# Kernel optimization log

Hardware: AMD Instinct MI355X
Metric: run time of the kernel (lower is better)

## Reference

```python
import jax, jax.numpy as jnp
import numpy as np

DIM = 1024
DIM_QK = 1024
DIM_V = 1024
H = 16
SCALE = 1.0 / (DIM_QK ** 0.5)  # NOTE: module scales by sqrt(dim_qk), not sqrt(head_dim)


def setup_inputs() -> dict:
    key = jax.random.key(0)
    ks = jax.random.split(key, 12)
    B, S = 2, 2048
    q = jax.random.normal(ks[0], (B, S, DIM), jnp.float32)
    k = jax.random.normal(ks[1], (B, S, DIM), jnp.float32)
    v = jax.random.normal(ks[2], (B, S, DIM), jnp.float32)
    mask = jax.random.randint(ks[3], (B, 1, S, S), 0, 2) > 0  # True = masked
    s = 1.0 / np.sqrt(DIM)
    Wq = jax.random.uniform(ks[4], (DIM_QK, DIM), jnp.float32, -s, s)
    bq = jax.random.uniform(ks[5], (DIM_QK,), jnp.float32, -s, s)
    Wk = jax.random.uniform(ks[6], (DIM_QK, DIM), jnp.float32, -s, s)
    bk = jax.random.uniform(ks[7], (DIM_QK,), jnp.float32, -s, s)
    Wv = jax.random.uniform(ks[8], (DIM_V, DIM), jnp.float32, -s, s)
    bv = jax.random.uniform(ks[9], (DIM_V,), jnp.float32, -s, s)
    Wo = jax.random.uniform(ks[10], (DIM_V, DIM), jnp.float32, -s, s)
    bo = jax.random.uniform(ks[11], (DIM_V,), jnp.float32, -s, s)
    return {"q": q, "k": k, "v": v, "mask": mask,
            "Wq": Wq, "bq": bq, "Wk": Wk, "bk": bk,
            "Wv": Wv, "bv": bv, "Wo": Wo, "bo": bo}


def reference(q, k, v, mask, Wq, bq, Wk, bk, Wv, bv, Wo, bo):
    B, Sq, _ = q.shape
    Skv = k.shape[1]
    # projections (torch Linear: x @ W.T + b)
    qh = (q @ Wq.T + bq).reshape(B, Sq, H, DIM_QK // H).transpose(0, 2, 1, 3)   # [B,H,Sq,dk]
    kh = (k @ Wk.T + bk).reshape(B, Skv, H, DIM_QK // H).transpose(0, 2, 1, 3)  # [B,H,Skv,dk]
    vh = (v @ Wv.T + bv).reshape(B, Skv, H, DIM_V // H).transpose(0, 2, 1, 3)   # [B,H,Skv,dv]
    attn = jnp.einsum('bhqd,bhkd->bhqk', qh, kh) * SCALE
    attn = jnp.where(mask, jnp.float32(-1e20), attn)
    attn = jax.nn.softmax(attn, axis=-1)
    # dropout is identity in eval / p=0
    out = jnp.einsum('bhqk,bhkd->bhqd', attn, vh)            # [B,H,Sq,dv]
    out = out.transpose(0, 2, 1, 3).reshape(B, Sq, DIM_V)
    return out @ Wo.T + bo
```

## Files before the change

kernel.cpp:

```cpp
#include <hip/hip_runtime.h>
#include <hip/hip_bf16.h>

typedef __attribute__((ext_vector_type(8))) __bf16 bf16x8;
typedef __attribute__((ext_vector_type(4))) short short4v;
typedef __attribute__((ext_vector_type(4))) float f32x4;
typedef __attribute__((ext_vector_type(4))) unsigned int uint4v;
typedef __attribute__((ext_vector_type(2))) unsigned int uint2v;

#define S_LEN 2048
#define DIM_  1024
#define HDIM  64
#define SCALE2 0.045084441f

#define EXP2F(x) __builtin_amdgcn_exp2f(x)

#define ATTN_SWZ(row, col8) (((row) * 64) + (((col8) ^ ((row) & 7)) << 3))

__device__ __forceinline__ void async_copy16(const void* gp, void* lp) {
  __builtin_amdgcn_global_load_lds(
      (const __attribute__((address_space(1))) unsigned int*)gp,
      (__attribute__((address_space(3))) unsigned int*)lp, 16, 0, 0);
}

__device__ __forceinline__ unsigned f2bf_u(float f) {
  unsigned u = __builtin_bit_cast(unsigned, f);
  return (u + 0x7FFFu + ((u >> 16) & 1u)) >> 16;
}
__device__ __forceinline__ unsigned pack2(float a, float b) {
  return f2bf_u(a) | (f2bf_u(b) << 16);
}
__device__ __forceinline__ unsigned cvtpk(float a, float b) {
  float2 f; f.x = a; f.y = b;
  __hip_bfloat162 h = __float22bfloat162_rn(f);
  unsigned u;
  __builtin_memcpy(&u, &h, 4);
  return u;
}

__global__ __launch_bounds__(256) void cvt_kernel(
    const float* __restrict__ s0, const float* __restrict__ s1, const float* __restrict__ s2,
    const float* __restrict__ s3, const float* __restrict__ s4, const float* __restrict__ s5,
    const float* __restrict__ s6,
    __hip_bfloat16* __restrict__ d0, __hip_bfloat16* __restrict__ d1, __hip_bfloat16* __restrict__ d2,
    __hip_bfloat16* __restrict__ d3, __hip_bfloat16* __restrict__ d4, __hip_bfloat16* __restrict__ d5,
    __hip_bfloat16* __restrict__ d6,
    const int* __restrict__ mask, unsigned long long* __restrict__ bits)
{
  if (blockIdx.y == 7) {
    int wave = threadIdx.x >> 6, lane = threadIdx.x & 63;
    int gw = blockIdx.x * 4 + wave;
#pragma unroll
    for (int it = 0; it < 16; ++it) {
      int w = gw * 16 + it;
      int m = mask[(size_t)w * 64 + lane];
      unsigned long long bal = __ballot(m != 0);
      if (lane == 0) bits[w] = bal;
    }
    return;
  }
  const float* srcs[7] = {s0, s1, s2, s3, s4, s5, s6};
  __hip_bfloat16* dsts[7] = {d0, d1, d2, d3, d4, d5, d6};
  const int sizes[7] = {4194304, 4194304, 4194304, 1048576, 1048576, 1048576, 1048576};
  int rg = blockIdx.y;
  int base = (blockIdx.x * 256 + threadIdx.x) * 8;
  if (base >= sizes[rg]) return;
  const float* s = srcs[rg] + base;
  f32x4 a = *(const f32x4*)s;
  f32x4 b = *(const f32x4*)(s + 4);
  uint4v o;
  o.x = pack2(a[0], a[1]); o.y = pack2(a[2], a[3]);
  o.z = pack2(b[0], b[1]); o.w = pack2(b[2], b[3]);
  *(uint4v*)(dsts[rg] + base) = o;
}

__device__ __forceinline__ void swz(int r, int& m0, int& n0) {
  int c  = ((r & 7) << 2) | (r >> 6);
  int xl = (r >> 3) & 7;
  m0 = ((c >> 3) * 8 + xl) * 128;
  n0 = (c & 7) * 128;
}

__global__ __launch_bounds__(256) void qkv_gemm_kernel(
    const __hip_bfloat16* __restrict__ xq, const __hip_bfloat16* __restrict__ xk,
    const __hip_bfloat16* __restrict__ xv,
    const __hip_bfloat16* __restrict__ Wq, const float* __restrict__ bq,
    const __hip_bfloat16* __restrict__ Wk, const float* __restrict__ bk,
    const __hip_bfloat16* __restrict__ Wv, const float* __restrict__ bv,
    __hip_bfloat16* __restrict__ Q, __hip_bfloat16* __restrict__ Kk,
    __hip_bfloat16* __restrict__ VT)
{
  const __hip_bfloat16 *X, *W; const float* bias;
  if (blockIdx.z == 0)      { X = xq; W = Wq; bias = bq; }
  else if (blockIdx.z == 1) { X = xk; W = Wk; bias = bk; }
  else                      { X = xv; W = Wv; bias = bv; }

  constexpr int K = 1024, N = 1024;
  __shared__ alignas(16) __hip_bfloat16 As[2][128 * 32];
  __shared__ alignas(16) __hip_bfloat16 Bs[2][128 * 32];
  const int tid  = threadIdx.x;
  const int lane = tid & 63;
  const int wave = tid >> 6;
  const int t    = lane & 15;
  const int quad = lane >> 4;
  const int wm   = wave >> 1;
  const int wn   = wave & 1;
  int m0, n0;
  swz(blockIdx.x, m0, n0);

  f32x4 acc[4][4] = {};

  const int c0 = tid, c1 = 256 + tid;
  const int r0 = c0 >> 2, o0 = (c0 & 3) * 8;
  const int r1 = c1 >> 2, o1 = (c1 & 3) * 8;
  const __hip_bfloat16* xp0 = &X[(size_t)(m0 + r0) * K + o0];
  const __hip_bfloat16* xp1 = &X[(size_t)(m0 + r1) * K + o1];
  const __hip_bfloat16* wp0 = &W[(size_t)(n0 + r0) * K + o0];
  const __hip_bfloat16* wp1 = &W[(size_t)(n0 + r1) * K + o1];

  async_copy16(xp0, &As[0][c0 * 8]);
  async_copy16(xp1, &As[0][c1 * 8]);
  async_copy16(wp0, &Bs[0][c0 * 8]);
  async_copy16(wp1, &Bs[0][c1 * 8]);

  int buf = 0;
  for (int k0 = 0; k0 < K; k0 += 32) {
    __syncthreads();
    if (k0 + 32 < K) {
      int nb = buf ^ 1;
      int kn = k0 + 32;
      async_copy16(xp0 + kn, &As[nb][c0 * 8]);
      async_copy16(xp1 + kn, &As[nb][c1 * 8]);
      async_copy16(wp0 + kn, &Bs[nb][c0 * 8]);
      async_copy16(wp1 + kn, &Bs[nb][c1 * 8]);
    }
    bf16x8 a[4], b[4];
#pragma unroll
    for (int i = 0; i < 4; ++i)
      a[i] = *(const bf16x8*)&As[buf][(wm * 64 + i * 16 + t) * 32 + quad * 8];
#pragma unroll
    for (int j = 0; j < 4; ++j)
      b[j] = *(const bf16x8*)&Bs[buf][(wn * 64 + j * 16 + t) * 32 + quad * 8];
#pragma unroll
    for (int i = 0; i < 4; ++i)
#pragma unroll
      for (int j = 0; j < 4; ++j)
        acc[i][j] = __builtin_amdgcn_mfma_f32_16x16x32_bf16(a[i], b[j], acc[i][j], 0, 0, 0);
    buf ^= 1;
  }

  float bj[4];
#pragma unroll
  for (int j = 0; j < 4; ++j)
    bj[j] = bias[n0 + wn * 64 + j * 16 + t];

  if (blockIdx.z == 2) {
#pragma unroll
    for (int i = 0; i < 4; ++i)
#pragma unroll
      for (int j = 0; j < 4; ++j) {
        int m = m0 + wm * 64 + i * 16 + quad * 4;
        int n = n0 + wn * 64 + j * 16 + t;
        int bb = m >> 11, kv = m & 2047;
        int hh = n >> 6,  dv = n & 63;
        uint2v o;
        o.x = pack2(acc[i][j][0] + bj[j], acc[i][j][1] + bj[j]);
        o.y = pack2(acc[i][j][2] + bj[j], acc[i][j][3] + bj[j]);
        *(uint2v*)&VT[(size_t)(((bb * 16 + hh) * 64) + dv) * 2048 + kv] = o;
      }
  } else {
    const bool isq = (blockIdx.z == 0);
    __hip_bfloat16* Out = isq ? Q : Kk;
    const float sc = isq ? SCALE2 : 1.0f;
#pragma unroll
    for (int i = 0; i < 4; ++i)
#pragma unroll
      for (int j = 0; j < 4; ++j)
#pragma unroll
        for (int r = 0; r < 4; ++r) {
          int m = m0 + wm * 64 + i * 16 + quad * 4 + r;
          int n = n0 + wn * 64 + j * 16 + t;
          Out[(size_t)m * N + n] = __float2bfloat16((acc[i][j][r] + bj[j]) * sc);
        }
  }
}

__global__ __launch_bounds__(256) void proj_gemm_kernel(
    const __hip_bfloat16* __restrict__ X, const __hip_bfloat16* __restrict__ W,
    const float* __restrict__ bias, float* __restrict__ Out)
{
  constexpr int K = 1024, N = 1024;
  __shared__ alignas(16) __hip_bfloat16 As[2][128 * 32];
  __shared__ alignas(16) __hip_bfloat16 Bs[2][128 * 32];
  const int tid  = threadIdx.x;
  const int lane = tid & 63;
  const int wave = tid >> 6;
  const int t    = lane & 15;
  const int quad = lane >> 4;
  const int wm   = wave >> 1;
  const int wn   = wave & 1;
  int m0, n0;
  swz(blockIdx.x, m0, n0);

  f32x4 acc[4][4] = {};

  const int c0 = tid, c1 = 256 + tid;
  const int r0 = c0 >> 2, o0 = (c0 & 3) * 8;
  const int r1 = c1 >> 2, o1 = (c1 & 3) * 8;
  const __hip_bfloat16* xp0 = &X[(size_t)(m0 + r0) * K + o0];
  const __hip_bfloat16* xp1 = &X[(size_t)(m0 + r1) * K + o1];
  const __hip_bfloat16* wp0 = &W[(size_t)(n0 + r0) * K + o0];
  const __hip_bfloat16* wp1 = &W[(size_t)(n0 + r1) * K + o1];

  async_copy16(xp0, &As[0][c0 * 8]);
  async_copy16(xp1, &As[0][c1 * 8]);
  async_copy16(wp0, &Bs[0][c0 * 8]);
  async_copy16(wp1, &Bs[0][c1 * 8]);

  int buf = 0;
  for (int k0 = 0; k0 < K; k0 += 32) {
    __syncthreads();
    if (k0 + 32 < K) {
      int nb = buf ^ 1;
      int kn = k0 + 32;
      async_copy16(xp0 + kn, &As[nb][c0 * 8]);
      async_copy16(xp1 + kn, &As[nb][c1 * 8]);
      async_copy16(wp0 + kn, &Bs[nb][c0 * 8]);
      async_copy16(wp1 + kn, &Bs[nb][c1 * 8]);
    }
    bf16x8 a[4], b[4];
#pragma unroll
    for (int i = 0; i < 4; ++i)
      a[i] = *(const bf16x8*)&As[buf][(wm * 64 + i * 16 + t) * 32 + quad * 8];
#pragma unroll
    for (int j = 0; j < 4; ++j)
      b[j] = *(const bf16x8*)&Bs[buf][(wn * 64 + j * 16 + t) * 32 + quad * 8];
#pragma unroll
    for (int i = 0; i < 4; ++i)
#pragma unroll
      for (int j = 0; j < 4; ++j)
        acc[i][j] = __builtin_amdgcn_mfma_f32_16x16x32_bf16(a[i], b[j], acc[i][j], 0, 0, 0);
    buf ^= 1;
  }

  float bj[4];
#pragma unroll
  for (int j = 0; j < 4; ++j)
    bj[j] = bias[n0 + wn * 64 + j * 16 + t];
#pragma unroll
  for (int i = 0; i < 4; ++i)
#pragma unroll
    for (int j = 0; j < 4; ++j)
#pragma unroll
      for (int r = 0; r < 4; ++r) {
        int m = m0 + wm * 64 + i * 16 + quad * 4 + r;
        int n = n0 + wn * 64 + j * 16 + t;
        Out[(size_t)m * N + n] = acc[i][j][r] + bj[j];
      }
}

__global__ __launch_bounds__(256) void attn_kernel(
    const __hip_bfloat16* __restrict__ Qb,
    const __hip_bfloat16* __restrict__ Kb,
    const __hip_bfloat16* __restrict__ VT,
    const unsigned long long* __restrict__ mbits,
    __hip_bfloat16* __restrict__ Ob)
{
  const int bid = blockIdx.x;
  const int qt = (bid >> 3) & 15;
  const int g  = ((bid & 7) << 2) | (bid >> 7);
  const int h  = g & 15;
  const int b  = g >> 4;
  const int qb = qt * 128;

  __shared__ alignas(16) __hip_bfloat16 Qs[128 * 64];
  __shared__ alignas(16) __hip_bfloat16 Ks[2][64 * 64];
  __shared__ alignas(16) __hip_bfloat16 Vt[2][64 * 64];

  const int tid  = threadIdx.x;
  const int lane = tid & 63;
  const int wave = tid >> 6;
  const int t    = lane & 15;
  const int quad = lane >> 4;

  const int r0 = tid >> 3;
  const int r1 = 32 + r0;
  const int k0c = ((tid & 7) ^ (r0 & 7)) << 3;
  const int k1c = ((tid & 7) ^ (r1 & 7)) << 3;
  const __hip_bfloat16* kp0 = &Kb[((size_t)(b * S_LEN + r0)) * DIM_ + h * HDIM + k0c];
  const __hip_bfloat16* kp1 = &Kb[((size_t)(b * S_LEN + r1)) * DIM_ + h * HDIM + k1c];
  const size_t vtbase = (size_t)((b * 16 + h) * 64) * 2048;
  const __hip_bfloat16* vp0 = &VT[vtbase + (size_t)r0 * 2048 + k0c];
  const __hip_bfloat16* vp1 = &VT[vtbase + (size_t)r1 * 2048 + k1c];

  async_copy16(kp0, &Ks[0][tid * 8]);
  async_copy16(kp1, &Ks[0][(256 + tid) * 8]);
  async_copy16(vp0, &Vt[0][tid * 8]);
  async_copy16(vp1, &Vt[0][(256 + tid) * 8]);

#pragma unroll
  for (int r = 0; r < 4; ++r) {
    int c = r * 256 + tid;
    int row = c >> 3, c8 = c & 7;
    uint4 raw = *(const uint4*)&Qb[((size_t)(b * S_LEN + qb + row)) * DIM_ + h * HDIM + c8 * 8];
    *(uint4*)&Qs[ATTN_SWZ(row, c8)] = raw;
  }
  __syncthreads();

  bf16x8 qf[2][2];
#pragma unroll
  for (int hh = 0; hh < 2; ++hh)
#pragma unroll
    for (int ks = 0; ks < 2; ++ks)
      qf[hh][ks] = *(const bf16x8*)&Qs[ATTN_SWZ(wave * 32 + hh * 16 + t, ks * 4 + quad)];

  int koff[8];
#pragma unroll
  for (int i = 0; i < 4; ++i) {
    koff[i]     = ATTN_SWZ(i * 16 + t, quad);
    koff[4 + i] = ATTN_SWZ(i * 16 + t, 4 + quad);
  }
  int voff[16];
#pragma unroll
  for (int j = 0; j < 4; ++j)
#pragma unroll
    for (int n = 0; n < 4; ++n)
      voff[j * 4 + n] = (n * 16 + t) * 64 +
          (((j * 2 + (quad >> 1)) ^ (t & 7)) << 3) + (quad & 1) * 4;

  f32x4 lpa = {0.f, 0.f, 0.f, 0.f};
  f32x4 lpb = {0.f, 0.f, 0.f, 0.f};
  f32x4 oa[4] = {};
  f32x4 ob[4] = {};

  const size_t mbase0 = ((size_t)b * S_LEN + qb + wave * 32 + t) * 32;
  const size_t mbase1 = mbase0 + 16 * 32;
  const int qshift = quad * 4;

#define ATTN_TILE(kvt, BUF)                                                   \
  {                                                                           \
    unsigned long long mw0 = mbits[mbase0 + (kvt)];                           \
    unsigned long long mw1 = mbits[mbase1 + (kvt)];                           \
    if ((kvt) > 0) __syncthreads();                \
    if ((kvt) + 1 < 32) {                                                     \
      size_t koffg = (size_t)((kvt) + 1) * 64 * DIM_;                         \
      int    voffg = ((kvt) + 1) * 64;                                        \
      async_copy16(kp0 + koffg, &Ks[(BUF) ^ 1][tid * 8]);                     \
      async_copy16(kp1 + koffg, &Ks[(BUF) ^ 1][(256 + tid) * 8]);             \
      async_copy16(vp0 + voffg, &Vt[(BUF) ^ 1][tid * 8]);                     \
      async_copy16(vp1 + voffg, &Vt[(BUF) ^ 1][(256 + tid) * 8]);             \
    }                                                                         \
    __builtin_amdgcn_s_setprio(1);                                            \
    unsigned long long mwq0 = mw0 >> qshift;                                  \
    unsigned long long mwq1 = mw1 >> qshift;                                  \
    unsigned m0lo = (unsigned)mwq0, m0hi = (unsigned)(mwq0 >> 32);            \
    unsigned m1lo = (unsigned)mwq1, m1hi = (unsigned)(mwq1 >> 32);            \
    unsigned mqv0[4] = {m0lo & 0xFu, (m0lo >> 16) & 0xFu,                     \
                        m0hi & 0xFu, (m0hi >> 16) & 0xFu};                    \
    unsigned mqv1[4] = {m1lo & 0xFu, (m1lo >> 16) & 0xFu,                     \
                        m1hi & 0xFu, (m1hi >> 16) & 0xFu};                    \
    bf16x8 kf[8];                                                             \
    _Pragma("unroll")                                                         \
    for (int i = 0; i < 4; ++i) {                                             \
      kf[i]     = *(const bf16x8*)&Ks[BUF][koff[i]];                          \
      kf[4 + i] = *(const bf16x8*)&Ks[BUF][koff[4 + i]];                      \
    }                                                                         \
    short4v pf0[4], pf1[4];                                                   \
    _Pragma("unroll")                                                         \
    for (int i = 0; i < 4; ++i) {                                             \
      f32x4 z = {};                                                           \
      z = __builtin_amdgcn_mfma_f32_16x16x32_bf16(kf[i], qf[0][0], z, 0, 0, 0);\
      z = __builtin_amdgcn_mfma_f32_16x16x32_bf16(kf[4 + i], qf[0][1], z, 0, 0, 0);\
      float e0, e1, e2, e3;                                                   \
      e0 = EXP2F((mqv0[i] & 1u) ? -1e20f : z[0]);                             \
      e1 = EXP2F((mqv0[i] & 2u) ? -1e20f : z[1]);                             \
      e2 = EXP2F((mqv0[i] & 4u) ? -1e20f : z[2]);                             \
      e3 = EXP2F((mqv0[i] & 8u) ? -1e20f : z[3]);                             \
      lpa[0] += e0; lpa[1] += e1; lpa[2] += e2; lpa[3] += e3;                 \
      uint2v pk;                                                              \
      pk.x = cvtpk(e0, e1);                                                   \
      pk.y = cvtpk(e2, e3);                                                   \
      pf0[i] = __builtin_bit_cast(short4v, pk);                               \
    }                                                                         \
    _Pragma("unroll")                                                         \
    for (int i = 0; i < 4; ++i) {                                             \
      f32x4 z = {};                                                           \
      z = __builtin_amdgcn_mfma_f32_16x16x32_bf16(kf[i], qf[1][0], z, 0, 0, 0);\
      z = __builtin_amdgcn_mfma_f32_16x16x32_bf16(kf[4 + i], qf[1][1], z, 0, 0, 0);\
      float e0, e1, e2, e3;                                                   \
      e0 = EXP2F((mqv1[i] & 1u) ? -1e20f : z[0]);                             \
      e1 = EXP2F((mqv1[i] & 2u) ? -1e20f : z[1]);                             \
      e2 = EXP2F((mqv1[i] & 4u) ? -1e20f : z[2]);                             \
      e3 = EXP2F((mqv1[i] & 8u) ? -1e20f : z[3]);                             \
      lpb[0] += e0; lpb[1] += e1; lpb[2] += e2; lpb[3] += e3;                 \
      uint2v pk;                                                              \
      pk.x = cvtpk(e0, e1);                                                   \
      pk.y = cvtpk(e2, e3);                                                   \
      pf1[i] = __builtin_bit_cast(short4v, pk);                               \
    }                                                                         \
    _Pragma("unroll")                                                         \
    for (int j = 0; j < 4; ++j)                                               \
      _Pragma("unroll")                                                       \
      for (int n = 0; n < 4; ++n) {                                           \
        short4v va = *(const short4v*)&Vt[BUF][voff[j * 4 + n]];              \
        oa[n] = __builtin_amdgcn_mfma_f32_16x16x16bf16_1k(va, pf0[j], oa[n],  \
                                                          0, 0, 0);           \
        ob[n] = __builtin_amdgcn_mfma_f32_16x16x16bf16_1k(va, pf1[j], ob[n],  \
                                                          0, 0, 0);           \
      }                                                                       \
    __builtin_amdgcn_s_setprio(0);                                            \
  }

  ATTN_TILE(0, 0)
  for (int kvt = 1; kvt < 31; kvt += 2) {
    ATTN_TILE(kvt, 1)
    ATTN_TILE(kvt + 1, 0)
  }
  ATTN_TILE(31, 1)
#undef ATTN_TILE

  float la = (lpa[0] + lpa[1]) + (lpa[2] + lpa[3]);
  la += __shfl_xor(la, 16, 64);
  la += __shfl_xor(la, 32, 64);
  float rla = 1.0f / la;
  float lb = (lpb[0] + lpb[1]) + (lpb[2] + lpb[3]);
  lb += __shfl_xor(lb, 16, 64);
  lb += __shfl_xor(lb, 32, 64);
  float rlb = 1.0f / lb;

  __hip_bfloat16* Ts = Qs;
  __syncthreads();
#pragma unroll
  for (int n = 0; n < 4; ++n) {
    int cswz = (((n * 2 + (quad >> 1)) ^ (t & 7)) << 3) + (quad & 1) * 4;
    uint2v pk;
    pk.x = cvtpk(oa[n][0] * rla, oa[n][1] * rla);
    pk.y = cvtpk(oa[n][2] * rla, oa[n][3] * rla);
    *(uint2v*)&Ts[(wave * 32 + t) * 64 + cswz] = pk;
    uint2v pk2;
    pk2.x = cvtpk(ob[n][0] * rlb, ob[n][1] * rlb);
    pk2.y = cvtpk(ob[n][2] * rlb, ob[n][3] * rlb);
    *(uint2v*)&Ts[(wave * 32 + 16 + t) * 64 + cswz] = pk2;
  }
  __syncthreads();
  {
    int row = tid >> 1;
    int half = tid & 1;
    __hip_bfloat16* dst = &Ob[((size_t)(b * S_LEN + qb + row)) * DIM_ + h * HDIM + half * 32];
#pragma unroll
    for (int bb = 0; bb < 4; ++bb) {
      int blk = half * 4 + bb;
      uint4 x = *(const uint4*)&Ts[row * 64 + ((blk ^ (row & 7)) << 3)];
      *(uint4*)(dst + bb * 8) = x;
    }
  }
}

extern "C" void kernel_launch(void* const* d_in, const int* in_sizes, int n_in,
                              void* d_out, int out_size, void* d_ws, size_t ws_size,
                              hipStream_t stream) {
  const float* q  = (const float*)d_in[0];
  const float* k  = (const float*)d_in[1];
  const float* v  = (const float*)d_in[2];
  const int*   mk = (const int*)d_in[3];
  const float* Wq = (const float*)d_in[4];
  const float* bq = (const float*)d_in[5];
  const float* Wk = (const float*)d_in[6];
  const float* bk = (const float*)d_in[7];
  const float* Wv = (const float*)d_in[8];
  const float* bv = (const float*)d_in[9];
  const float* Wo = (const float*)d_in[10];
  const float* bo = (const float*)d_in[11];
  float* out = (float*)d_out;

  char* ws = (char*)d_ws;
  const size_t MB = 1024 * 1024;
  __hip_bfloat16* Qb  = (__hip_bfloat16*)(ws);
  __hip_bfloat16* Kb  = (__hip_bfloat16*)(ws + 8  * MB);
  __hip_bfloat16* VTb = (__hip_bfloat16*)(ws + 16 * MB);
  __hip_bfloat16* Ob  = (__hip_bfloat16*)(ws + 24 * MB);
  __hip_bfloat16* xqb = (__hip_bfloat16*)(ws + 32 * MB);
  __hip_bfloat16* xkb = (__hip_bfloat16*)(ws + 40 * MB);
  __hip_bfloat16* xvb = (__hip_bfloat16*)(ws + 48 * MB);
  __hip_bfloat16* Wqb = (__hip_bfloat16*)(ws + 56 * MB);
  __hip_bfloat16* Wkb = (__hip_bfloat16*)(ws + 58 * MB);
  __hip_bfloat16* Wvb = (__hip_bfloat16*)(ws + 60 * MB);
  __hip_bfloat16* Wob = (__hip_bfloat16*)(ws + 62 * MB);
  unsigned long long* mbits = (unsigned long long*)(ws + 64 * MB);

  cvt_kernel<<<dim3(2048, 8), 256, 0, stream>>>(q, k, v, Wq, Wk, Wv, Wo,
                                                xqb, xkb, xvb, Wqb, Wkb, Wvb, Wob,
                                                mk, mbits);
  qkv_gemm_kernel<<<dim3(256, 1, 3), 256, 0, stream>>>(xqb, xkb, xvb,
                                                       Wqb, bq, Wkb, bk, Wvb, bv,
                                                       Qb, Kb, VTb);
  attn_kernel<<<dim3(512), 256, 0, stream>>>(Qb, Kb, VTb, mbits, Ob);
  proj_gemm_kernel<<<dim3(256), 256, 0, stream>>>(Ob, Wob, bo, out);
}
```

Before: 264.0 us.

## Triple-buffer K/V tiles with explicit vmcnt waits and prefetch mask bits

Moves the attention K/V staging from double to triple buffering, so loads for tile kvt+2 are issued while tile kvt is computed. The __syncthreads per tile becomes an explicit s_waitcnt vmcnt plus s_barrier, which lets later loads stay in flight instead of draining every outstanding load. The mask bit words are also loaded one tile ahead. In exchange the block uses more LDS, which may lower occupancy, and the hand-counted vmcnt values must match the exact number of outstanding loads to stay correct.

```diff
diff --git a/kernel.cpp b/kernel.cpp
--- a/kernel.cpp
+++ b/kernel.cpp
@@ -273,8 +273,8 @@
   const int qb = qt * 128;
 
   __shared__ alignas(16) __hip_bfloat16 Qs[128 * 64];
-  __shared__ alignas(16) __hip_bfloat16 Ks[2][64 * 64];
-  __shared__ alignas(16) __hip_bfloat16 Vt[2][64 * 64];
+  __shared__ alignas(16) __hip_bfloat16 Ks[3][64 * 64];
+  __shared__ alignas(16) __hip_bfloat16 Vt[3][64 * 64];
 
   const int tid  = threadIdx.x;
   const int lane = tid & 63;
@@ -296,6 +296,13 @@
   async_copy16(kp1, &Ks[0][(256 + tid) * 8]);
   async_copy16(vp0, &Vt[0][tid * 8]);
   async_copy16(vp1, &Vt[0][(256 + tid) * 8]);
+  {
+    size_t ko = (size_t)64 * DIM_;
+    async_copy16(kp0 + ko, &Ks[1][tid * 8]);
+    async_copy16(kp1 + ko, &Ks[1][(256 + tid) * 8]);
+    async_copy16(vp0 + 64, &Vt[1][tid * 8]);
+    async_copy16(vp1 + 64, &Vt[1][(256 + tid) * 8]);
+  }
 
 #pragma unroll
   for (int r = 0; r < 4; ++r) {
@@ -304,6 +311,13 @@
     uint4 raw = *(const uint4*)&Qb[((size_t)(b * S_LEN + qb + row)) * DIM_ + h * HDIM + c8 * 8];
     *(uint4*)&Qs[ATTN_SWZ(row, c8)] = raw;
   }
+
+  const size_t mbase0 = ((size_t)b * S_LEN + qb + wave * 32 + t) * 32;
+  const size_t mbase1 = mbase0 + 16 * 32;
+  unsigned long long mc0 = mbits[mbase0];
+  unsigned long long mc1 = mbits[mbase1];
+  unsigned long long mn0, mn1;
+
   __syncthreads();
 
   bf16x8 qf[2][2];
@@ -332,26 +346,13 @@
   f32x4 oa[4] = {};
   f32x4 ob[4] = {};
 
-  const size_t mbase0 = ((size_t)b * S_LEN + qb + wave * 32 + t) * 32;
-  const size_t mbase1 = mbase0 + 16 * 32;
   const int qshift = quad * 4;
 
-#define ATTN_TILE(kvt, BUF)                                                   \
-  {                                                                           \
-    unsigned long long mw0 = mbits[mbase0 + (kvt)];                           \
-    unsigned long long mw1 = mbits[mbase1 + (kvt)];                           \
-    if ((kvt) > 0) __syncthreads();                \
-    if ((kvt) + 1 < 32) {                                                     \
-      size_t koffg = (size_t)((kvt) + 1) * 64 * DIM_;                         \
-      int    voffg = ((kvt) + 1) * 64;                                        \
-      async_copy16(kp0 + koffg, &Ks[(BUF) ^ 1][tid * 8]);                     \
-      async_copy16(kp1 + koffg, &Ks[(BUF) ^ 1][(256 + tid) * 8]);             \
-      async_copy16(vp0 + voffg, &Vt[(BUF) ^ 1][tid * 8]);                     \
-      async_copy16(vp1 + voffg, &Vt[(BUF) ^ 1][(256 + tid) * 8]);             \
-    }                                                                         \
+#define COMPUTE_TILE(B)                                                       \
     __builtin_amdgcn_s_setprio(1);                                            \
-    unsigned long long mwq0 = mw0 >> qshift;                                  \
-    unsigned long long mwq1 = mw1 >> qshift;                                  \
+    {                                                                         \
+    unsigned long long mwq0 = mc0 >> qshift;                                  \
+    unsigned long long mwq1 = mc1 >> qshift;                                  \
     unsigned m0lo = (unsigned)mwq0, m0hi = (unsigned)(mwq0 >> 32);            \
     unsigned m1lo = (unsigned)mwq1, m1hi = (unsigned)(mwq1 >> 32);            \
     unsigned mqv0[4] = {m0lo & 0xFu, (m0lo >> 16) & 0xFu,                     \
@@ -361,8 +362,8 @@
     bf16x8 kf[8];                                                             \
     _Pragma("unroll")                                                         \
     for (int i = 0; i < 4; ++i) {                                             \
-      kf[i]     = *(const bf16x8*)&Ks[BUF][koff[i]];                          \
-      kf[4 + i] = *(const bf16x8*)&Ks[BUF][koff[4 + i]];                      \
+      kf[i]     = *(const bf16x8*)&Ks[B][koff[i]];                            \
+      kf[4 + i] = *(const bf16x8*)&Ks[B][koff[4 + i]];                        \
     }                                                                         \
     short4v pf0[4], pf1[4];                                                   \
     _Pragma("unroll")                                                         \
@@ -401,22 +402,66 @@
     for (int j = 0; j < 4; ++j)                                               \
       _Pragma("unroll")                                                       \
       for (int n = 0; n < 4; ++n) {                                           \
-        short4v va = *(const short4v*)&Vt[BUF][voff[j * 4 + n]];              \
+        short4v va = *(const short4v*)&Vt[B][voff[j * 4 + n]];                \
         oa[n] = __builtin_amdgcn_mfma_f32_16x16x16bf16_1k(va, pf0[j], oa[n],  \
                                                           0, 0, 0);           \
         ob[n] = __builtin_amdgcn_mfma_f32_16x16x16bf16_1k(va, pf1[j], ob[n],  \
                                                           0, 0, 0);           \
       }                                                                       \
-    __builtin_amdgcn_s_setprio(0);                                            \
-  }
-
-  ATTN_TILE(0, 0)
-  for (int kvt = 1; kvt < 31; kvt += 2) {
-    ATTN_TILE(kvt, 1)
-    ATTN_TILE(kvt + 1, 0)
-  }
-  ATTN_TILE(31, 1)
+    }                                                                         \
+    __builtin_amdgcn_s_setprio(0);
+
+#define STAGE_TILE(kvt, BN)                                                   \
+    {                                                                         \
+      size_t koffg = (size_t)(kvt) * 64 * DIM_;                               \
+      int    voffg = (kvt) * 64;                                              \
+      async_copy16(kp0 + koffg, &Ks[BN][tid * 8]);                            \
+      async_copy16(kp1 + koffg, &Ks[BN][(256 + tid) * 8]);                    \
+      async_copy16(vp0 + voffg, &Vt[BN][tid * 8]);                            \
+      async_copy16(vp1 + voffg, &Vt[BN][(256 + tid) * 8]);                    \
+    }
+
+#define ATTN_TILE(kvt, B, BN, VMS)                                            \
+  {                                                                           \
+    asm volatile("s_waitcnt vmcnt(" VMS ")" ::: "memory");                    \
+    __builtin_amdgcn_s_barrier();                                             \
+    STAGE_TILE((kvt) + 2, BN)                                                 \
+    mn0 = mbits[mbase0 + (kvt) + 1];                                          \
+    mn1 = mbits[mbase1 + (kvt) + 1];                                          \
+    COMPUTE_TILE(B)                                                           \
+    mc0 = mn0; mc1 = mn1;                                                     \
+  }
+
+  {
+    STAGE_TILE(2, 2)
+    mn0 = mbits[mbase0 + 1];
+    mn1 = mbits[mbase1 + 1];
+    COMPUTE_TILE(0)
+    mc0 = mn0; mc1 = mn1;
+  }
+  for (int kvt = 1; kvt < 28; kvt += 3) {
+    ATTN_TILE(kvt,     1, 0, "6")
+    ATTN_TILE(kvt + 1, 2, 1, "6")
+    ATTN_TILE(kvt + 2, 0, 2, "6")
+  }
+  ATTN_TILE(28, 1, 0, "6")
+  ATTN_TILE(29, 2, 1, "6")
+  {
+    asm volatile("s_waitcnt vmcnt(6)" ::: "memory");
+    __builtin_amdgcn_s_barrier();
+    mn0 = mbits[mbase0 + 31];
+    mn1 = mbits[mbase1 + 31];
+    COMPUTE_TILE(0)
+    mc0 = mn0; mc1 = mn1;
+  }
+  {
+    asm volatile("s_waitcnt vmcnt(2)" ::: "memory");
+    __builtin_amdgcn_s_barrier();
+    COMPUTE_TILE(1)
+  }
 #undef ATTN_TILE
+#undef STAGE_TILE
+#undef COMPUTE_TILE
 
   float la = (lpa[0] + lpa[1]) + (lpa[2] + lpa[3]);
   la += __shfl_xor(la, 16, 64);
```

After: 295.5 us. 1.12x slower.
